# Kernel optimization log

Measured on AMD Instinct MI355X. Metric: run time of the kernel, lower is better.

## Reference

```python
import jax, jax.numpy as jnp
import numpy as np

CHANNELS = 512
GROUPS = 32
EPS = 1e-5


def setup_inputs() -> dict:
    key = jax.random.key(0)
    ks = jax.random.split(key, 7)
    C = CHANNELS
    x = jax.random.normal(ks[0], (32, C, 32, 32), dtype=jnp.float32)
    norm_w = jax.random.normal(ks[1], (C,), dtype=jnp.float32) * 0.02 + 1.0
    norm_b = jax.random.normal(ks[2], (C,), dtype=jnp.float32) * 0.02
    # 1x1 convs stored as (out_channels, in_channels)
    qkv_w = jax.random.normal(ks[3], (3 * C, C), dtype=jnp.float32) * (C ** -0.5)
    qkv_b = jax.random.normal(ks[4], (3 * C,), dtype=jnp.float32) * 0.02
    proj_w = jax.random.normal(ks[5], (C, C), dtype=jnp.float32) * (C ** -0.5)
    proj_b = jax.random.normal(ks[6], (C,), dtype=jnp.float32) * 0.02
    return {"x": x, "norm_w": norm_w, "norm_b": norm_b,
            "qkv_w": qkv_w, "qkv_b": qkv_b,
            "proj_w": proj_w, "proj_b": proj_b}


def _group_norm(x, w, b):
    B, C, H, W = x.shape
    xg = x.reshape(B, GROUPS, C // GROUPS, H, W)
    mean = xg.mean(axis=(2, 3, 4), keepdims=True)
    var = xg.var(axis=(2, 3, 4), keepdims=True)
    xn = ((xg - mean) * jax.lax.rsqrt(var + EPS)).reshape(B, C, H, W)
    return xn * w[None, :, None, None] + b[None, :, None, None]


def reference(x, norm_w, norm_b, qkv_w, qkv_b, proj_w, proj_b):
    B, C, H, W = x.shape
    scale = C ** (-0.5)
    h = _group_norm(x, norm_w, norm_b)
    # 1x1 conv == per-pixel linear: (B,C,H,W) -> (B,3C,H,W)
    qkv = jnp.einsum('bchw,oc->bohw', h, qkv_w) + qkv_b[None, :, None, None]
    qkv = qkv.reshape(B, 3, C, H * W)
    q, k, v = qkv[:, 0], qkv[:, 1], qkv[:, 2]  # each (B, C, N)
    # attn[b, i, j] = softmax_j( q[:, i] . k[:, j] * scale )
    scores = jnp.einsum('bcn,bcm->bnm', q, k) * scale  # (B, N, N)
    attn = jax.nn.softmax(scores, axis=-1)
    # h[b, c, i] = sum_j v[b, c, j] * attn[b, i, j]
    hout = jnp.einsum('bcm,bnm->bcn', v, attn).reshape(B, C, H, W)
    out = x + jnp.einsum('bchw,oc->bohw', hout, proj_w) + proj_b[None, :, None, None]
    return out
```

## Files before the change

kernel.cpp:

```cpp
#include <hip/hip_runtime.h>
#include <math.h>

#define B_ 32
#define C_ 512
#define G_ 32
#define N_ 1024
#define OC3_ 1536
#define EPS_ 1e-5f

typedef __attribute__((ext_vector_type(8))) short short8;
typedef __attribute__((ext_vector_type(4))) float f32x4;

__device__ inline unsigned short f2bf(float f) {
    unsigned u = __builtin_bit_cast(unsigned, f);
    u += 0x7fffu + ((u >> 16) & 1u);
    return (unsigned short)(u >> 16);
}
__device__ inline unsigned pack2(float lo, float hi) {
    return (unsigned)f2bf(lo) | ((unsigned)f2bf(hi) << 16);
}
__device__ inline float bf2f(unsigned short u) {
    return __builtin_bit_cast(float, ((unsigned)u) << 16);
}

typedef const __attribute__((address_space(1))) unsigned int* gas_u32;
typedef __attribute__((address_space(3))) unsigned int* las_u32;
__device__ __forceinline__ void cp16(unsigned short* lds, const unsigned short* g) {
    __builtin_amdgcn_global_load_lds((gas_u32)g, (las_u32)lds, 16, 0, 0);
}

__device__ __forceinline__ void xcd_decode(int bid, int nbpb, int nbz,
                                           int& bz, int& local) {
    if ((nbz & 7) == 0) {
        int xcd = bid & 7;
        int rest = bid >> 3;
        local = rest % nbpb;
        bz = (rest / nbpb) * 8 + xcd;
    } else {
        bz = bid / nbpb;
        local = bid % nbpb;
    }
}

__global__ __launch_bounds__(256) void gn_stats_kernel(
    const float* __restrict__ x, float* __restrict__ stats)
{
    int bg = blockIdx.x;
    const float4* xv = (const float4*)(x + (size_t)bg * 16 * N_);
    float s = 0.f, ss = 0.f;
    for (int i = threadIdx.x; i < 4096; i += 256) {
        float4 v = xv[i];
        s  += v.x + v.y + v.z + v.w;
        ss += v.x*v.x + v.y*v.y + v.z*v.z + v.w*v.w;
    }
    __shared__ float r1[256], r2[256];
    r1[threadIdx.x] = s; r2[threadIdx.x] = ss;
    __syncthreads();
    for (int off = 128; off > 0; off >>= 1) {
        if (threadIdx.x < off) {
            r1[threadIdx.x] += r1[threadIdx.x + off];
            r2[threadIdx.x] += r2[threadIdx.x + off];
        }
        __syncthreads();
    }
    if (threadIdx.x == 0) {
        float mean = r1[0] * (1.f / 16384.f);
        float var  = r2[0] * (1.f / 16384.f) - mean * mean;
        stats[bg * 2 + 0] = mean;
        stats[bg * 2 + 1] = rsqrtf(var + EPS_);
    }
}

__global__ __launch_bounds__(256) void cvt_bf16_kernel(
    const float* __restrict__ src, unsigned short* __restrict__ dst, int n4)
{
    int i = blockIdx.x * 256 + threadIdx.x;
    if (i >= n4) return;
    float4 v = ((const float4*)src)[i];
    uint2 o; o.x = pack2(v.x, v.y); o.y = pack2(v.z, v.w);
    ((uint2*)dst)[i] = o;
}

__global__ __launch_bounds__(256) void hhatT_kernel(
    const float* __restrict__ x, const float* __restrict__ stats,
    const float* __restrict__ nw, const float* __restrict__ nbias,
    unsigned short* __restrict__ hhatT, long sH, int b0, int nbz)
{
    int bz, local;
    xcd_decode(blockIdx.x, 128, nbz, bz, local);
    int b = b0 + bz;
    int nt = (local & 15) * 64, ct = (local >> 4) * 64;
    const float* xb = x + (size_t)b * C_ * N_;
    const float* st = stats + b * 2 * G_;

    __shared__ float T[64][65];
    int tid = threadIdx.x;

    #pragma unroll
    for (int p = 0; p < 4; ++p) {
        int c = p * 16 + (tid >> 4);
        int n4 = (tid & 15) * 4;
        float4 v = *(const float4*)&xb[(size_t)(ct + c) * N_ + nt + n4];
        int g = (ct + c) >> 4;
        float w0 = nw[ct + c] * st[g * 2 + 1];
        float bb = nbias[ct + c] - st[g * 2] * w0;
        T[c][n4]   = v.x * w0 + bb;
        T[c][n4+1] = v.y * w0 + bb;
        T[c][n4+2] = v.z * w0 + bb;
        T[c][n4+3] = v.w * w0 + bb;
    }
    __syncthreads();
    #pragma unroll
    for (int p = 0; p < 2; ++p) {
        int n  = p * 32 + (tid >> 3);
        int c8 = (tid & 7) * 8;
        short8 s;
        #pragma unroll
        for (int u = 0; u < 8; ++u) s[u] = (short)f2bf(T[c8 + u][n]);
        *(short8*)&hhatT[(size_t)bz * sH + (size_t)(nt + n) * C_ + ct + c8] = s;
    }
}

template<int EPI>
__global__ __launch_bounds__(256) void gemm128(
    const unsigned short* __restrict__ A, long sA, int lda,
    const unsigned short* __restrict__ B, long sB, int ldb,
    void* __restrict__ Dv, long sD, int ldd,
    const float* __restrict__ bias,
    const float* __restrict__ aux, long sAux,
    int K, float scale, int gx, int gy, int nbz)
{
    int bz, local;
    xcd_decode(blockIdx.x, gx * gy, nbz, bz, local);

    int bx, by;
    bool p2 = false;
    if constexpr (EPI == 5) {
        p2 = local >= 64;
        int li = p2 ? local - 64 : local;
        bx = p2 ? (li & 3) : (li & 7);
        by = p2 ? (li >> 2) : (li >> 3);
    } else {
        bx = local % gx;
        by = local / gx;
    }

    const unsigned short *Ab, *Bb;
    if constexpr (EPI == 5) {
        if (p2) {
            Ab = B + (size_t)(1024 + bx * 128) * ldb;
            Bb = A + (size_t)bz * sA + (size_t)by * 128 * lda;
        } else {
            Ab = A + (size_t)bz * sA + (size_t)bx * 128 * lda;
            Bb = B + (size_t)by * 128 * ldb;
        }
    } else {
        Ab = A + (size_t)bz * sA + (size_t)bx * 128 * lda;
        Bb = B + (size_t)bz * sB + (size_t)by * 128 * ldb;
    }

    __shared__ __align__(16) unsigned short smem[4][4096];

    int tid = threadIdx.x;
    int w = tid >> 6, lane = tid & 63;
    int lm = lane & 15, q = lane >> 4;
    int wrow = (w >> 1) * 64, wcol = (w & 1) * 64;

    f32x4 acc[4][4];
    #pragma unroll
    for (int i = 0; i < 4; ++i)
        #pragma unroll
        for (int j = 0; j < 4; ++j) acc[i][j] = (f32x4)(0.f);

    int srow = tid >> 2;
    int skc  = (((tid & 3) ^ ((tid >> 3) & 3))) * 8;
    int fco  = (q ^ ((lm >> 1) & 3)) * 8;

    const unsigned short* a0p = Ab + (size_t)srow        * lda + skc;
    const unsigned short* a1p = Ab + (size_t)(64 + srow) * lda + skc;
    const unsigned short* b0p = Bb + (size_t)srow        * ldb + skc;
    const unsigned short* b1p = Bb + (size_t)(64 + srow) * ldb + skc;

    cp16(&smem[0][tid * 8],        a0p);
    cp16(&smem[0][2048 + tid * 8], a1p);
    cp16(&smem[2][tid * 8],        b0p);
    cp16(&smem[2][2048 + tid * 8], b1p);

    int nIter = K >> 5;
    for (int it = 0; it < nIter; ++it) {
        int cur = it & 1;
        __syncthreads();
        if (it + 1 < nIter) {
            int off = (it + 1) * 32;
            int nxt = cur ^ 1;
            cp16(&smem[nxt][tid * 8],            a0p + off);
            cp16(&smem[nxt][2048 + tid * 8],     a1p + off);
            cp16(&smem[2 + nxt][tid * 8],        b0p + off);
            cp16(&smem[2 + nxt][2048 + tid * 8], b1p + off);
        }
        short8 af[4], bf[4];
        #pragma unroll
        for (int i = 0; i < 4; ++i)
            af[i] = *(const short8*)&smem[cur][(wrow + i * 16 + lm) * 32 + fco];
        #pragma unroll
        for (int j = 0; j < 4; ++j)
            bf[j] = *(const short8*)&smem[2 + cur][(wcol + j * 16 + lm) * 32 + fco];
        #pragma unroll
        for (int i = 0; i < 4; ++i)
            #pragma unroll
            for (int j = 0; j < 4; ++j)
                acc[i][j] = __builtin_amdgcn_mfma_f32_16x16x32_bf16(
                    af[i], bf[j], acc[i][j], 0, 0, 0);
    }

    __syncthreads();

    if constexpr (EPI != 4) {
        unsigned short* Ts = &smem[0][0];
        #pragma unroll
        for (int j = 0; j < 4; ++j) {
            int lc = wcol + j * 16 + lm;
            float cb = 0.f;
            if constexpr (EPI == 5) { if (!p2) cb = bias[by * 128 + lc]; }
            #pragma unroll
            for (int i = 0; i < 4; ++i) {
                #pragma unroll
                for (int r = 0; r < 4; ++r) {
                    int lr = wrow + i * 16 + q * 4 + r;
                    float vle = acc[i][j][r];
                    if constexpr (EPI == 2) vle *= scale;
                    else if constexpr (EPI == 5)
                        vle += p2 ? bias[1024 + bx * 128 + lr] : cb;
                    int wkey = (lr >> 2) & 7;
                    Ts[lr * 128 + (lc ^ (wkey << 3))] = f2bf(vle);
                }
            }
        }
        __syncthreads();
        size_t doff = 0;
        if constexpr (EPI == 5) { if (p2) doff = (size_t)(1u << 20); }
        unsigned short* Dp = (unsigned short*)Dv + doff +
            (size_t)bz * sD + (size_t)(bx * 128) * ldd + by * 128;
        #pragma unroll
        for (int k = 0; k < 8; ++k) {
            int flat = k * 2048 + tid * 8;
            int rr = flat >> 7, cc = flat & 127;
            int key = (rr >> 2) & 7;
            short8 vv = *(const short8*)&Ts[flat ^ (key << 3)];
            *(short8*)&Dp[(size_t)rr * ldd + cc] = vv;
        }
    } else {
        float* Ts32 = (float*)&smem[0][0];
        float* Dp = (float*)Dv + (size_t)bz * sD + (size_t)(bx * 128) * ldd + by * 128;
        const float* Ap = aux + (size_t)bz * sAux + (size_t)(bx * 128) * ldd + by * 128;
        #pragma unroll
        for (int h = 0; h < 2; ++h) {
            if (h) __syncthreads();
            if ((w & 1) == h) {
                #pragma unroll
                for (int j = 0; j < 4; ++j) {
                    int lch = j * 16 + lm;
                    #pragma unroll
                    for (int i = 0; i < 4; ++i) {
                        #pragma unroll
                        for (int r = 0; r < 4; ++r) {
                            int lr = wrow + i * 16 + q * 4 + r;
                            int wkey = (lr >> 2) & 7;
                            Ts32[lr * 64 + (lch ^ (wkey << 3))] =
                                acc[i][j][r] + bias[bx * 128 + lr];
                        }
                    }
                }
            }
            __syncthreads();
            #pragma unroll
            for (int k = 0; k < 8; ++k) {
                int flat = k * 1024 + tid * 4;
                int rr = flat >> 6, cc = flat & 63;
                int key = (rr >> 2) & 7;
                f32x4 vv = *(const f32x4*)&Ts32[flat ^ (key << 3)];
                size_t go = (size_t)rr * ldd + h * 64 + cc;
                f32x4 av = *(const f32x4*)&Ap[go];
                *(f32x4*)&Dp[go] = vv + av;
            }
        }
    }
}

__global__ __launch_bounds__(256) void softmax_kernel(
    unsigned short* __restrict__ sc, long sSc, int nbz)
{
    int bz, local;
    xcd_decode(blockIdx.x, 256, nbz, bz, local);
    int row = local * 4 + (threadIdx.x >> 6);
    int lane = threadIdx.x & 63;
    unsigned short* p = sc + (size_t)bz * sSc + (size_t)row * N_ + lane * 16;

    short8 s0 = *(const short8*)p;
    short8 s1 = *(const short8*)(p + 8);
    float v[16];
    #pragma unroll
    for (int i = 0; i < 8; ++i) {
        v[i]     = bf2f((unsigned short)s0[i]);
        v[8 + i] = bf2f((unsigned short)s1[i]);
    }
    float m = v[0];
    #pragma unroll
    for (int i = 1; i < 16; ++i) m = fmaxf(m, v[i]);
    #pragma unroll
    for (int off = 32; off > 0; off >>= 1) m = fmaxf(m, __shfl_xor(m, off, 64));

    float sum = 0.f;
    #pragma unroll
    for (int i = 0; i < 16; ++i) { v[i] = __expf(v[i] - m); sum += v[i]; }
    #pragma unroll
    for (int off = 32; off > 0; off >>= 1) sum += __shfl_xor(sum, off, 64);
    float inv = 1.f / sum;

    short8 o0, o1;
    #pragma unroll
    for (int i = 0; i < 8; ++i) {
        o0[i] = (short)f2bf(v[i] * inv);
        o1[i] = (short)f2bf(v[8 + i] * inv);
    }
    *(short8*)p = o0;
    *(short8*)(p + 8) = o1;
}

extern "C" void kernel_launch(void* const* d_in, const int* in_sizes, int n_in,
                              void* d_out, int out_size, void* d_ws, size_t ws_size,
                              hipStream_t stream) {
    const float* x      = (const float*)d_in[0];
    const float* norm_w = (const float*)d_in[1];
    const float* norm_b = (const float*)d_in[2];
    const float* qkv_w  = (const float*)d_in[3];
    const float* qkv_b  = (const float*)d_in[4];
    const float* proj_w = (const float*)d_in[5];
    const float* proj_b = (const float*)d_in[6];
    float* out = (float*)d_out;

    char* ws = (char*)d_ws;
    float* stats = (float*)ws;
    unsigned short* wqkv  = (unsigned short*)(ws + 8192);
    unsigned short* wproj = wqkv + (size_t)OC3_ * C_;
    char* base = (char*)(wproj + (size_t)C_ * C_);
    const size_t fixed = 8192 + (size_t)OC3_ * C_ * 2 + (size_t)C_ * C_ * 2;

    const size_t REG = 6u << 20;
    const long RSH = (long)(REG / 2);

    size_t avail = ws_size > fixed ? ws_size - fixed : 0;
    int chunk = (int)(avail / REG);
    if (chunk < 1) chunk = 1;
    if (chunk > B_) chunk = B_;

    gn_stats_kernel<<<dim3(B_ * G_), dim3(256), 0, stream>>>(x, stats);
    cvt_bf16_kernel<<<dim3((OC3_ * C_ / 4 + 255) / 256), dim3(256), 0, stream>>>(
        qkv_w, wqkv, OC3_ * C_ / 4);
    cvt_bf16_kernel<<<dim3((C_ * C_ / 4 + 255) / 256), dim3(256), 0, stream>>>(
        proj_w, wproj, C_ * C_ / 4);

    const float scale = 0.044194173824159216f;

    unsigned short* qkT   = (unsigned short*)base;
    unsigned short* vbuf  = (unsigned short*)(base + (2u << 20));
    unsigned short* hhatT = (unsigned short*)(base + (3u << 20));
    unsigned short* houtT = (unsigned short*)(base + (3u << 20));
    unsigned short* sc    = (unsigned short*)(base + (4u << 20));

    for (int b0 = 0; b0 < B_; b0 += chunk) {
        int nb = B_ - b0 < chunk ? B_ - b0 : chunk;

        hhatT_kernel<<<dim3(128 * nb), dim3(256), 0, stream>>>(
            x, stats, norm_w, norm_b, hhatT, RSH, b0, nb);

        gemm128<5><<<dim3(96 * nb), dim3(256), 0, stream>>>(
            hhatT, RSH, C_,  wqkv, 0, C_,
            qkT, RSH, 1024,  qkv_b, nullptr, 0, C_, 0.f, 96, 1, nb);

        gemm128<2><<<dim3(8 * 8 * nb), dim3(256), 0, stream>>>(
            qkT, RSH, 1024,  qkT + 512, RSH, 1024,
            sc, RSH, N_,  nullptr, nullptr, 0, C_, scale, 8, 8, nb);

        softmax_kernel<<<dim3(256 * nb), dim3(256), 0, stream>>>(sc, RSH, nb);

        gemm128<3><<<dim3(8 * 4 * nb), dim3(256), 0, stream>>>(
            sc, RSH, N_,  vbuf, RSH, N_,
            houtT, RSH, C_,  nullptr, nullptr, 0, N_, 0.f, 8, 4, nb);

        gemm128<4><<<dim3(4 * 8 * nb), dim3(256), 0, stream>>>(
            wproj, 0, C_,  houtT, RSH, C_,
            out + (size_t)b0 * C_ * N_, (long)C_ * N_, N_,
            proj_b, x + (size_t)b0 * C_ * N_, (long)C_ * N_, C_, 0.f, 4, 8, nb);
    }
}
```

Before: 385.2 us.

## Widen GEMM tiles to 128x256 and merge prep kernels into one launch

All four batched GEMMs move from 128x128 to 128x256 output tiles. Each wave now holds a 64x128 accumulator (32 MFMA tiles) and the B operand tile in LDS is doubled, which reuses each A fragment across more MFMAs and halves the grid sizes. The epilogues are reworked to drain the larger tile in halves or quarters through LDS with new swizzles. The group-norm stats kernel and the two weight bf16 conversions are merged into a single prep kernel to save launches. The risks are higher register pressure, fewer blocks per launch on a 256-CU device, and more LDS per block.

```diff
diff --git a/kernel.cpp b/kernel.cpp
--- a/kernel.cpp
+++ b/kernel.cpp
@@ -42,43 +42,53 @@
     }
 }
 
-__global__ __launch_bounds__(256) void gn_stats_kernel(
-    const float* __restrict__ x, float* __restrict__ stats)
+__global__ __launch_bounds__(256) void prep_kernel(
+    const float* __restrict__ x, float* __restrict__ stats,
+    const float* __restrict__ qkv_w, unsigned short* __restrict__ wqkv,
+    const float* __restrict__ proj_w, unsigned short* __restrict__ wproj)
 {
-    int bg = blockIdx.x;
-    const float4* xv = (const float4*)(x + (size_t)bg * 16 * N_);
-    float s = 0.f, ss = 0.f;
-    for (int i = threadIdx.x; i < 4096; i += 256) {
-        float4 v = xv[i];
-        s  += v.x + v.y + v.z + v.w;
-        ss += v.x*v.x + v.y*v.y + v.z*v.z + v.w*v.w;
-    }
     __shared__ float r1[256], r2[256];
-    r1[threadIdx.x] = s; r2[threadIdx.x] = ss;
-    __syncthreads();
-    for (int off = 128; off > 0; off >>= 1) {
-        if (threadIdx.x < off) {
-            r1[threadIdx.x] += r1[threadIdx.x + off];
-            r2[threadIdx.x] += r2[threadIdx.x + off];
-        }
+    int bid = blockIdx.x;
+    if (bid < 1024) {
+        int bg = bid;
+        const float4* xv = (const float4*)(x + (size_t)bg * 16 * N_);
+        float s = 0.f, ss = 0.f;
+        for (int i = threadIdx.x; i < 4096; i += 256) {
+            float4 v = xv[i];
+            s  += v.x + v.y + v.z + v.w;
+            ss += v.x*v.x + v.y*v.y + v.z*v.z + v.w*v.w;
+        }
+        r1[threadIdx.x] = s; r2[threadIdx.x] = ss;
         __syncthreads();
-    }
-    if (threadIdx.x == 0) {
-        float mean = r1[0] * (1.f / 16384.f);
-        float var  = r2[0] * (1.f / 16384.f) - mean * mean;
-        stats[bg * 2 + 0] = mean;
-        stats[bg * 2 + 1] = rsqrtf(var + EPS_);
-    }
-}
-
-__global__ __launch_bounds__(256) void cvt_bf16_kernel(
-    const float* __restrict__ src, unsigned short* __restrict__ dst, int n4)
-{
-    int i = blockIdx.x * 256 + threadIdx.x;
-    if (i >= n4) return;
-    float4 v = ((const float4*)src)[i];
-    uint2 o; o.x = pack2(v.x, v.y); o.y = pack2(v.z, v.w);
-    ((uint2*)dst)[i] = o;
+        for (int off = 128; off > 0; off >>= 1) {
+            if (threadIdx.x < off) {
+                r1[threadIdx.x] += r1[threadIdx.x + off];
+                r2[threadIdx.x] += r2[threadIdx.x + off];
+            }
+            __syncthreads();
+        }
+        if (threadIdx.x == 0) {
+            float mean = r1[0] * (1.f / 16384.f);
+            float var  = r2[0] * (1.f / 16384.f) - mean * mean;
+            stats[bg * 2 + 0] = mean;
+            stats[bg * 2 + 1] = rsqrtf(var + EPS_);
+        }
+    } else {
+        int i = (bid - 1024) * 256 + threadIdx.x;
+        const int nQ = OC3_ * C_ / 4;
+        float4 v;
+        uint2 o;
+        if (i < nQ) {
+            v = ((const float4*)qkv_w)[i];
+            o.x = pack2(v.x, v.y); o.y = pack2(v.z, v.w);
+            ((uint2*)wqkv)[i] = o;
+        } else {
+            int j = i - nQ;
+            v = ((const float4*)proj_w)[j];
+            o.x = pack2(v.x, v.y); o.y = pack2(v.z, v.w);
+            ((uint2*)wproj)[j] = o;
+        }
+    }
 }
 
 __global__ __launch_bounds__(256) void hhatT_kernel(
@@ -122,7 +132,7 @@
 }
 
 template<int EPI>
-__global__ __launch_bounds__(256) void gemm128(
+__global__ __launch_bounds__(256) void gemmk(
     const unsigned short* __restrict__ A, long sA, int lda,
     const unsigned short* __restrict__ B, long sB, int ldb,
     void* __restrict__ Dv, long sD, int ldd,
@@ -136,8 +146,8 @@
     int bx, by;
     bool p2 = false;
     if constexpr (EPI == 5) {
-        p2 = local >= 64;
-        int li = p2 ? local - 64 : local;
+        p2 = local >= 32;
+        int li = p2 ? local - 32 : local;
         bx = p2 ? (li & 3) : (li & 7);
         by = p2 ? (li >> 2) : (li >> 3);
     } else {
@@ -149,28 +159,30 @@
     if constexpr (EPI == 5) {
         if (p2) {
             Ab = B + (size_t)(1024 + bx * 128) * ldb;
-            Bb = A + (size_t)bz * sA + (size_t)by * 128 * lda;
+            Bb = A + (size_t)bz * sA + (size_t)by * 256 * lda;
         } else {
             Ab = A + (size_t)bz * sA + (size_t)bx * 128 * lda;
-            Bb = B + (size_t)by * 128 * ldb;
+            Bb = B + (size_t)by * 256 * ldb;
         }
     } else {
         Ab = A + (size_t)bz * sA + (size_t)bx * 128 * lda;
-        Bb = B + (size_t)bz * sB + (size_t)by * 128 * ldb;
-    }
-
-    __shared__ __align__(16) unsigned short smem[4][4096];
+        Bb = B + (size_t)bz * sB + (size_t)by * 256 * ldb;
+    }
+
+    __shared__ __align__(16) unsigned short smem[24576];
+    #define AS_(c) (smem + (c) * 4096)
+    #define BS_(c) (smem + 8192 + (c) * 8192)
 
     int tid = threadIdx.x;
     int w = tid >> 6, lane = tid & 63;
     int lm = lane & 15, q = lane >> 4;
-    int wrow = (w >> 1) * 64, wcol = (w & 1) * 64;
-
-    f32x4 acc[4][4];
+    int wrow = (w >> 1) * 64, wcol = (w & 1) * 128;
+
+    f32x4 acc[4][8];
     #pragma unroll
     for (int i = 0; i < 4; ++i)
         #pragma unroll
-        for (int j = 0; j < 4; ++j) acc[i][j] = (f32x4)(0.f);
+        for (int j = 0; j < 8; ++j) acc[i][j] = (f32x4)(0.f);
 
     int srow = tid >> 2;
     int skc  = (((tid & 3) ^ ((tid >> 3) & 3))) * 8;
@@ -178,13 +190,16 @@
 
     const unsigned short* a0p = Ab + (size_t)srow        * lda + skc;
     const unsigned short* a1p = Ab + (size_t)(64 + srow) * lda + skc;
-    const unsigned short* b0p = Bb + (size_t)srow        * ldb + skc;
-    const unsigned short* b1p = Bb + (size_t)(64 + srow) * ldb + skc;
-
-    cp16(&smem[0][tid * 8],        a0p);
-    cp16(&smem[0][2048 + tid * 8], a1p);
-    cp16(&smem[2][tid * 8],        b0p);
-    cp16(&smem[2][2048 + tid * 8], b1p);
+    const unsigned short* bp[4];
+    #pragma unroll
+    for (int s = 0; s < 4; ++s)
+        bp[s] = Bb + (size_t)(s * 64 + srow) * ldb + skc;
+
+    cp16(AS_(0) + tid * 8,        a0p);
+    cp16(AS_(0) + 2048 + tid * 8, a1p);
+    #pragma unroll
+    for (int s = 0; s < 4; ++s)
+        cp16(BS_(0) + s * 2048 + tid * 8, bp[s]);
 
     int nIter = K >> 5;
     for (int it = 0; it < nIter; ++it) {
@@ -193,22 +208,23 @@
         if (it + 1 < nIter) {
             int off = (it + 1) * 32;
             int nxt = cur ^ 1;
-            cp16(&smem[nxt][tid * 8],            a0p + off);
-            cp16(&smem[nxt][2048 + tid * 8],     a1p + off);
-            cp16(&smem[2 + nxt][tid * 8],        b0p + off);
-            cp16(&smem[2 + nxt][2048 + tid * 8], b1p + off);
-        }
-        short8 af[4], bf[4];
+            cp16(AS_(nxt) + tid * 8,        a0p + off);
+            cp16(AS_(nxt) + 2048 + tid * 8, a1p + off);
+            #pragma unroll
+            for (int s = 0; s < 4; ++s)
+                cp16(BS_(nxt) + s * 2048 + tid * 8, bp[s] + off);
+        }
+        short8 af[4], bf[8];
         #pragma unroll
         for (int i = 0; i < 4; ++i)
-            af[i] = *(const short8*)&smem[cur][(wrow + i * 16 + lm) * 32 + fco];
-        #pragma unroll
-        for (int j = 0; j < 4; ++j)
-            bf[j] = *(const short8*)&smem[2 + cur][(wcol + j * 16 + lm) * 32 + fco];
+            af[i] = *(const short8*)&AS_(cur)[(wrow + i * 16 + lm) * 32 + fco];
+        #pragma unroll
+        for (int j = 0; j < 8; ++j)
+            bf[j] = *(const short8*)&BS_(cur)[(wcol + j * 16 + lm) * 32 + fco];
         #pragma unroll
         for (int i = 0; i < 4; ++i)
             #pragma unroll
-            for (int j = 0; j < 4; ++j)
+            for (int j = 0; j < 8; ++j)
                 acc[i][j] = __builtin_amdgcn_mfma_f32_16x16x32_bf16(
                     af[i], bf[j], acc[i][j], 0, 0, 0);
     }
@@ -216,50 +232,57 @@
     __syncthreads();
 
     if constexpr (EPI != 4) {
-        unsigned short* Ts = &smem[0][0];
-        #pragma unroll
-        for (int j = 0; j < 4; ++j) {
-            int lc = wcol + j * 16 + lm;
-            float cb = 0.f;
-            if constexpr (EPI == 5) { if (!p2) cb = bias[by * 128 + lc]; }
-            #pragma unroll
-            for (int i = 0; i < 4; ++i) {
-                #pragma unroll
-                for (int r = 0; r < 4; ++r) {
-                    int lr = wrow + i * 16 + q * 4 + r;
-                    float vle = acc[i][j][r];
-                    if constexpr (EPI == 2) vle *= scale;
-                    else if constexpr (EPI == 5)
-                        vle += p2 ? bias[1024 + bx * 128 + lr] : cb;
-                    int wkey = (lr >> 2) & 7;
-                    Ts[lr * 128 + (lc ^ (wkey << 3))] = f2bf(vle);
-                }
-            }
-        }
-        __syncthreads();
-        size_t doff = 0;
-        if constexpr (EPI == 5) { if (p2) doff = (size_t)(1u << 20); }
-        unsigned short* Dp = (unsigned short*)Dv + doff +
-            (size_t)bz * sD + (size_t)(bx * 128) * ldd + by * 128;
-        #pragma unroll
-        for (int k = 0; k < 8; ++k) {
-            int flat = k * 2048 + tid * 8;
-            int rr = flat >> 7, cc = flat & 127;
-            int key = (rr >> 2) & 7;
-            short8 vv = *(const short8*)&Ts[flat ^ (key << 3)];
-            *(short8*)&Dp[(size_t)rr * ldd + cc] = vv;
-        }
-    } else {
-        float* Ts32 = (float*)&smem[0][0];
-        float* Dp = (float*)Dv + (size_t)bz * sD + (size_t)(bx * 128) * ldd + by * 128;
-        const float* Ap = aux + (size_t)bz * sAux + (size_t)(bx * 128) * ldd + by * 128;
+        unsigned short* Ts = smem;
         #pragma unroll
         for (int h = 0; h < 2; ++h) {
             if (h) __syncthreads();
             if ((w & 1) == h) {
                 #pragma unroll
-                for (int j = 0; j < 4; ++j) {
-                    int lch = j * 16 + lm;
+                for (int j = 0; j < 8; ++j) {
+                    int lc = j * 16 + lm;
+                    float cb = 0.f;
+                    if constexpr (EPI == 5) {
+                        if (!p2) cb = bias[by * 256 + h * 128 + lc];
+                    }
+                    #pragma unroll
+                    for (int i = 0; i < 4; ++i) {
+                        #pragma unroll
+                        for (int r = 0; r < 4; ++r) {
+                            int lr = wrow + i * 16 + q * 4 + r;
+                            float vle = acc[i][j][r];
+                            if constexpr (EPI == 2) vle *= scale;
+                            else if constexpr (EPI == 5)
+                                vle += p2 ? bias[1024 + bx * 128 + lr] : cb;
+                            Ts[lr * 128 + (lc ^ (q << 4))] = f2bf(vle);
+                        }
+                    }
+                }
+            }
+            __syncthreads();
+            size_t doff = 0;
+            if constexpr (EPI == 5) { if (p2) doff = (size_t)(1u << 20); }
+            unsigned short* Dp = (unsigned short*)Dv + doff +
+                (size_t)bz * sD + (size_t)(bx * 128) * ldd + by * 256 + h * 128;
+            #pragma unroll
+            for (int k = 0; k < 8; ++k) {
+                int flat = k * 2048 + tid * 8;
+                int rr = flat >> 7, cc = flat & 127;
+                short8 vv = *(const short8*)&Ts[flat ^ (w << 4)];
+                *(short8*)&Dp[(size_t)rr * ldd + cc] = vv;
+            }
+        }
+    } else {
+        float* Ts32 = (float*)smem;
+        float* Dp = (float*)Dv + (size_t)bz * sD + (size_t)(bx * 128) * ldd + by * 256;
+        const float* Ap = aux + (size_t)bz * sAux + (size_t)(bx * 128) * ldd + by * 256;
+        #pragma unroll
+        for (int qd = 0; qd < 4; ++qd) {
+            if (qd) __syncthreads();
+            if ((w & 1) == (qd >> 1)) {
+                #pragma unroll
+                for (int jj = 0; jj < 4; ++jj) {
+                    int j = (qd & 1) * 4 + jj;
+                    int lch = jj * 16 + lm;
                     #pragma unroll
                     for (int i = 0; i < 4; ++i) {
                         #pragma unroll
@@ -277,14 +300,16 @@
             for (int k = 0; k < 8; ++k) {
                 int flat = k * 1024 + tid * 4;
                 int rr = flat >> 6, cc = flat & 63;
-                int key = (rr >> 2) & 7;
+                int key = (4 * k + w) & 7;
                 f32x4 vv = *(const f32x4*)&Ts32[flat ^ (key << 3)];
-                size_t go = (size_t)rr * ldd + h * 64 + cc;
+                size_t go = (size_t)rr * ldd + qd * 64 + cc;
                 f32x4 av = *(const f32x4*)&Ap[go];
                 *(f32x4*)&Dp[go] = vv + av;
             }
         }
     }
+    #undef AS_
+    #undef BS_
 }
 
 __global__ __launch_bounds__(256) void softmax_kernel(
@@ -354,11 +379,8 @@
     if (chunk < 1) chunk = 1;
     if (chunk > B_) chunk = B_;
 
-    gn_stats_kernel<<<dim3(B_ * G_), dim3(256), 0, stream>>>(x, stats);
-    cvt_bf16_kernel<<<dim3((OC3_ * C_ / 4 + 255) / 256), dim3(256), 0, stream>>>(
-        qkv_w, wqkv, OC3_ * C_ / 4);
-    cvt_bf16_kernel<<<dim3((C_ * C_ / 4 + 255) / 256), dim3(256), 0, stream>>>(
-        proj_w, wproj, C_ * C_ / 4);
+    prep_kernel<<<dim3(2048), dim3(256), 0, stream>>>(
+        x, stats, qkv_w, wqkv, proj_w, wproj);
 
     const float scale = 0.044194173824159216f;
 
@@ -374,23 +396,23 @@
         hhatT_kernel<<<dim3(128 * nb), dim3(256), 0, stream>>>(
             x, stats, norm_w, norm_b, hhatT, RSH, b0, nb);
 
-        gemm128<5><<<dim3(96 * nb), dim3(256), 0, stream>>>(
+        gemmk<5><<<dim3(48 * nb), dim3(256), 0, stream>>>(
             hhatT, RSH, C_,  wqkv, 0, C_,
-            qkT, RSH, 1024,  qkv_b, nullptr, 0, C_, 0.f, 96, 1, nb);
-
-        gemm128<2><<<dim3(8 * 8 * nb), dim3(256), 0, stream>>>(
+            qkT, RSH, 1024,  qkv_b, nullptr, 0, C_, 0.f, 48, 1, nb);
+
+        gemmk<2><<<dim3(8 * 4 * nb), dim3(256), 0, stream>>>(
             qkT, RSH, 1024,  qkT + 512, RSH, 1024,
-            sc, RSH, N_,  nullptr, nullptr, 0, C_, scale, 8, 8, nb);
+            sc, RSH, N_,  nullptr, nullptr, 0, C_, scale, 8, 4, nb);
 
         softmax_kernel<<<dim3(256 * nb), dim3(256), 0, stream>>>(sc, RSH, nb);
 
-        gemm128<3><<<dim3(8 * 4 * nb), dim3(256), 0, stream>>>(
+        gemmk<3><<<dim3(8 * 2 * nb), dim3(256), 0, stream>>>(
             sc, RSH, N_,  vbuf, RSH, N_,
-            houtT, RSH, C_,  nullptr, nullptr, 0, N_, 0.f, 8, 4, nb);
-
-        gemm128<4><<<dim3(4 * 8 * nb), dim3(256), 0, stream>>>(
+            houtT, RSH, C_,  nullptr, nullptr, 0, N_, 0.f, 8, 2, nb);
+
+        gemmk<4><<<dim3(4 * 4 * nb), dim3(256), 0, stream>>>(
             wproj, 0, C_,  houtT, RSH, C_,
             out + (size_t)b0 * C_ * N_, (long)C_ * N_, N_,
-            proj_b, x + (size_t)b0 * C_ * N_, (long)C_ * N_, C_, 0.f, 4, 8, nb);
-    }
-}
+            proj_b, x + (size_t)b0 * C_ * N_, (long)C_ * N_, C_, 0.f, 4, 4, nb);
+    }
+}
```

New measurement: 488.7 us. 1.27x slower.
